# Kernel tuning notes

Measured on AMD Instinct MI355X. Metric: run time of the kernel, lower is better.

The kernel has to match this reference:

```python
import jax, jax.numpy as jnp
import numpy as np

B, H, W_GRID, K = 1024, 64, 64, 10
NEG = -1e30
DIRS = ((-1, 0), (1, 0), (0, -1), (0, 1))


def _shift(x, di, dj):
    # out[..., i, j] = x[..., i+di, j+dj]; wrapped values are masked out later
    return jnp.roll(x, (-di, -dj), axis=(-2, -1))


def _valid_masks():
    ii = jnp.arange(H)[:, None]
    jj = jnp.arange(W_GRID)[None, :]
    return [(ii + di >= 0) & (ii + di < H) & (jj + dj >= 0) & (jj + dj < W_GRID)
            for di, dj in DIRS]


def setup_inputs() -> dict:
    key = jax.random.key(0)
    ks = jax.random.split(key, 8)
    walls = (jax.random.uniform(ks[0], (B, H, W_GRID)) < 0.2).astype(jnp.float32)
    aidx = jax.random.randint(ks[1], (B,), 0, H * W_GRID)
    agent = jnp.zeros((B, H * W_GRID), jnp.float32).at[jnp.arange(B), aidx].set(1.0)
    agent = agent.reshape(B, H, W_GRID)
    goal = (jax.random.uniform(ks[2], (B, H, W_GRID)) < 0.02).astype(jnp.float32)
    obs = jnp.stack([walls, agent, goal], axis=-1)  # [B,H,W,3]
    W_phi = jax.random.normal(ks[3], (3, 3), jnp.float32) * 0.5
    b_phi = jnp.zeros((3,), jnp.float32)
    W1 = jax.random.normal(ks[4], (36, 256), jnp.float32) / np.float32(np.sqrt(36.0))
    b1 = jnp.zeros((256,), jnp.float32)
    W2 = jax.random.normal(ks[5], (256, 256), jnp.float32) / np.float32(16.0)
    b2 = jnp.zeros((256,), jnp.float32)
    W_logits = jax.random.normal(ks[6], (256, 5), jnp.float32) * 0.01
    b_logits = jnp.zeros((5,), jnp.float32)
    return {"obs": obs, "W_phi": W_phi, "b_phi": b_phi, "W1": W1, "b1": b1,
            "W2": W2, "b2": b2, "W_logits": W_logits, "b_logits": b_logits}


def _forward(obs, W_phi, b_phi, W1, b1, W2, b2, W_logits, b_logits):
    # Phi: per-cell 3->3 linear + relu (original detaches phi before VP_nn)
    phi = jax.nn.relu(jnp.einsum('bhwc,cd->bhwd', obs, W_phi) + b_phi)
    phi = jax.lax.stop_gradient(phi)
    p, rin, rout = phi[..., 0], phi[..., 1], phi[..., 2]  # each [B,H,W]
    masks = _valid_masks()
    rin_sh = [_shift(rin, di, dj) for di, dj in DIRS]

    def step(v, _):
        best = v
        for m, rs, (di, dj) in zip(masks, rin_sh, DIRS):
            nv = p * _shift(v, di, dj) + rs - rout
            best = jnp.maximum(best, jnp.where(m, nv, NEG))
        return best, None

    v0 = jnp.zeros((B, H, W_GRID), phi.dtype)
    v, _ = jax.lax.scan(step, v0, None, length=K)  # final value map [B,H,W]

    # agent position = first nonzero / argmax of channel 1
    w_ch = 1.0 - obs[..., 0]  # forward flips wall channel before neighborhood
    a_ch = obs[..., 1]
    g_ch = obs[..., 2]
    flat = jnp.argmax(a_ch.reshape(B, -1), axis=1)
    r = flat // W_GRID
    c = flat % W_GRID

    def window(x, rr, cc):
        xp = jnp.pad(x, ((1, 1), (1, 1)))
        return jax.lax.dynamic_slice(xp, (rr, cc), (3, 3)).reshape(9)

    def per_sample(wc, ac, gc, vc, rr, cc):
        return jnp.concatenate([window(wc, rr, cc), window(ac, rr, cc),
                                window(gc, rr, cc), window(vc, rr, cc)])

    feats = jax.vmap(per_sample)(w_ch, a_ch, g_ch, v, r, c)  # [B,36]

    # hidden SlimFCs have activation_fn=None (linear), per SlimFC defaults
    h = feats @ W1 + b1
    h = h @ W2 + b2
    return h @ W_logits + b_logits  # [B,5]


def reference(obs, W_phi, b_phi, W1, b1, W2, b2, W_logits, b_logits):
    return _forward(obs, W_phi, b_phi, W1, b1, W2, b2, W_logits, b_logits)
```

## Files before the change

kernel.cpp:

```cpp
#include <hip/hip_runtime.h>


#define K_ITERS 10

__device__ __forceinline__ float shr1(float x) {
    return __int_as_float(__builtin_amdgcn_mov_dpp(__float_as_int(x), 0x138, 0xF, 0xF, true));
}
__device__ __forceinline__ float shl1(float x) {
    return __int_as_float(__builtin_amdgcn_mov_dpp(__float_as_int(x), 0x130, 0xF, 0xF, true));
}
__device__ __forceinline__ float max3(float a, float b, float c) {
    return fmaxf(fmaxf(a, b), c);
}

__global__ __launch_bounds__(512) void vin_fused_kernel(
    const float* __restrict__ obs,
    const float* __restrict__ W_phi,
    const float* __restrict__ b_phi,
    const float* __restrict__ W1,
    const float* __restrict__ b1,
    const float* __restrict__ W2,
    const float* __restrict__ b2,
    const float* __restrict__ Wl,
    const float* __restrict__ bl,
    float* __restrict__ out)
{
    const int b   = blockIdx.x;
    const int tid = threadIdx.x;
    const int w   = tid >> 6;
    const int l   = tid & 63;

    __shared__ float v_s[64 * 64];
    __shared__ float bndU[2][9][64];
    __shared__ float bndD[2][9][64];
    __shared__ float rbU[9][64];
    __shared__ float rbD[9][64];
    __shared__ int   agent_pos;
    __shared__ float f_s[36];
    __shared__ float part_s[2][256];
    __shared__ __align__(16) float h1_s[256];
    __shared__ float h2_s[256];
    __shared__ float red[8][5];

    const float* ob = obs + (size_t)b * (4096 * 3);

    const float w00 = W_phi[0], w01 = W_phi[1], w02 = W_phi[2];
    const float w10 = W_phi[3], w11 = W_phi[4], w12 = W_phi[5];
    const float w20 = W_phi[6], w21 = W_phi[7], w22 = W_phi[8];
    const float bp0 = b_phi[0], bp1 = b_phi[1], bp2 = b_phi[2];

    float pk[8], rik[8], rok[8];
    #pragma unroll
    for (int k = 0; k < 8; ++k) {
        const int cell = (8 * w + k) * 64 + l;
        const float o0 = ob[cell * 3 + 0];
        const float o1 = ob[cell * 3 + 1];
        const float o2 = ob[cell * 3 + 2];
        pk[k]  = fmaxf(fmaf(o2, w20, fmaf(o1, w10, fmaf(o0, w00, bp0))), 0.f);
        rik[k] = fmaxf(fmaf(o2, w21, fmaf(o1, w11, fmaf(o0, w01, bp1))), 0.f);
        rok[k] = fmaxf(fmaf(o2, w22, fmaf(o1, w12, fmaf(o0, w02, bp2))), 0.f);
        if (o1 > 0.5f) agent_pos = cell;
    }
    const float p0 = pk[0], p1 = pk[1], p2 = pk[2], p3 = pk[3];
    const float p4 = pk[4], p5 = pk[5], p6 = pk[6], p7 = pk[7];

    if (tid < 64) {
        bndU[0][0][l] = 0.f; bndU[1][0][l] = 0.f;
        bndD[0][8][l] = 0.f; bndD[1][8][l] = 0.f;
        rbU[0][l] = 0.f;     rbD[8][l] = 0.f;
    }
    rbU[w + 1][l] = rik[7];
    rbD[w][l]     = rik[0];
    __syncthreads();
    const float rinU_b = rbU[w][l];
    const float rinD_b = rbD[w + 1][l];

    const float aU0 = rinU_b - rok[0], aU1 = rik[0] - rok[1], aU2 = rik[1] - rok[2], aU3 = rik[2] - rok[3];
    const float aU4 = rik[3] - rok[4], aU5 = rik[4] - rok[5], aU6 = rik[5] - rok[6], aU7 = rik[6] - rok[7];
    const float aD0 = rik[1] - rok[0], aD1 = rik[2] - rok[1], aD2 = rik[3] - rok[2], aD3 = rik[4] - rok[3];
    const float aD4 = rik[5] - rok[4], aD5 = rik[6] - rok[5], aD6 = rik[7] - rok[6], aD7 = rinD_b - rok[7];
    const float aL0 = shr1(rik[0]) - rok[0], aL1 = shr1(rik[1]) - rok[1], aL2 = shr1(rik[2]) - rok[2], aL3 = shr1(rik[3]) - rok[3];
    const float aL4 = shr1(rik[4]) - rok[4], aL5 = shr1(rik[5]) - rok[5], aL6 = shr1(rik[6]) - rok[6], aL7 = shr1(rik[7]) - rok[7];
    const float aR0 = shl1(rik[0]) - rok[0], aR1 = shl1(rik[1]) - rok[1], aR2 = shl1(rik[2]) - rok[2], aR3 = shl1(rik[3]) - rok[3];
    const float aR4 = shl1(rik[4]) - rok[4], aR5 = shl1(rik[5]) - rok[5], aR6 = shl1(rik[6]) - rok[6], aR7 = shl1(rik[7]) - rok[7];

    float v0 = fmaxf(max3(aU0, aD0, aL0), fmaxf(aR0, 0.f));
    float v1 = fmaxf(max3(aU1, aD1, aL1), fmaxf(aR1, 0.f));
    float v2 = fmaxf(max3(aU2, aD2, aL2), fmaxf(aR2, 0.f));
    float v3 = fmaxf(max3(aU3, aD3, aL3), fmaxf(aR3, 0.f));
    float v4 = fmaxf(max3(aU4, aD4, aL4), fmaxf(aR4, 0.f));
    float v5 = fmaxf(max3(aU5, aD5, aL5), fmaxf(aR5, 0.f));
    float v6 = fmaxf(max3(aU6, aD6, aL6), fmaxf(aR6, 0.f));
    float v7 = fmaxf(max3(aU7, aD7, aL7), fmaxf(aR7, 0.f));
    bndU[0][w + 1][l] = v7;
    bndD[0][w][l]     = v0;

    #pragma unroll
    for (int it = 1; it < K_ITERS; ++it) {
        const int rd = (it - 1) & 1, wr = it & 1;
        __syncthreads();
        const float vU_b = bndU[rd][w][l];
        const float vD_b = bndD[rd][w + 1][l];

        float vL, vR, m;
        vL = shr1(v7); vR = shl1(v7);
        m = max3(fmaf(p7, v6, aU7), fmaf(p7, vD_b, aD7), fmaf(p7, vL, aL7));
        const float nv7 = max3(m, fmaf(p7, vR, aR7), v7);
        bndU[wr][w + 1][l] = nv7;

        vL = shr1(v0); vR = shl1(v0);
        m = max3(fmaf(p0, vU_b, aU0), fmaf(p0, v1, aD0), fmaf(p0, vL, aL0));
        const float nv0 = max3(m, fmaf(p0, vR, aR0), v0);
        bndD[wr][w][l] = nv0;

        vL = shr1(v1); vR = shl1(v1);
        m = max3(fmaf(p1, v0, aU1), fmaf(p1, v2, aD1), fmaf(p1, vL, aL1));
        const float nv1 = max3(m, fmaf(p1, vR, aR1), v1);

        vL = shr1(v2); vR = shl1(v2);
        m = max3(fmaf(p2, v1, aU2), fmaf(p2, v3, aD2), fmaf(p2, vL, aL2));
        const float nv2 = max3(m, fmaf(p2, vR, aR2), v2);

        vL = shr1(v3); vR = shl1(v3);
        m = max3(fmaf(p3, v2, aU3), fmaf(p3, v4, aD3), fmaf(p3, vL, aL3));
        const float nv3 = max3(m, fmaf(p3, vR, aR3), v3);

        vL = shr1(v4); vR = shl1(v4);
        m = max3(fmaf(p4, v3, aU4), fmaf(p4, v5, aD4), fmaf(p4, vL, aL4));
        const float nv4 = max3(m, fmaf(p4, vR, aR4), v4);

        vL = shr1(v5); vR = shl1(v5);
        m = max3(fmaf(p5, v4, aU5), fmaf(p5, v6, aD5), fmaf(p5, vL, aL5));
        const float nv5 = max3(m, fmaf(p5, vR, aR5), v5);

        vL = shr1(v6); vR = shl1(v6);
        m = max3(fmaf(p6, v5, aU6), fmaf(p6, v7, aD6), fmaf(p6, vL, aL6));
        const float nv6 = max3(m, fmaf(p6, vR, aR6), v6);

        v0 = nv0; v1 = nv1; v2 = nv2; v3 = nv3;
        v4 = nv4; v5 = nv5; v6 = nv6; v7 = nv7;
    }

    v_s[(8 * w + 0) * 64 + l] = v0;
    v_s[(8 * w + 1) * 64 + l] = v1;
    v_s[(8 * w + 2) * 64 + l] = v2;
    v_s[(8 * w + 3) * 64 + l] = v3;
    v_s[(8 * w + 4) * 64 + l] = v4;
    v_s[(8 * w + 5) * 64 + l] = v5;
    v_s[(8 * w + 6) * 64 + l] = v6;
    v_s[(8 * w + 7) * 64 + l] = v7;
    __syncthreads();

    if (tid < 36) {
        const int ap = agent_pos;
        const int ar = ap >> 6, ac = ap & 63;
        const int g  = tid / 9, o = tid % 9;
        const int rr = ar + o / 3 - 1;
        const int cc = ac + o % 3 - 1;
        float val = 0.f;
        if (rr >= 0 && rr < 64 && cc >= 0 && cc < 64) {
            const int cell = rr * 64 + cc;
            if      (g == 0) val = 1.f - ob[cell * 3 + 0];
            else if (g == 1) val = ob[cell * 3 + 1];
            else if (g == 2) val = ob[cell * 3 + 2];
            else             val = v_s[cell];
        }
        f_s[tid] = val;
    }
    __syncthreads();

    {
        const int h = tid >> 8;
        const int c = tid & 255;
        float a = 0.f;
        #pragma unroll
        for (int m = 0; m < 18; ++m) {
            const int i = 18 * h + m;
            a = fmaf(f_s[i], W1[i * 256 + c], a);
        }
        part_s[h][c] = a;
    }
    __syncthreads();
    if (tid < 256) h1_s[tid] = b1[tid] + part_s[0][tid] + part_s[1][tid];
    __syncthreads();

    {
        const int h = tid >> 8;
        const int c = tid & 255;
        float a = 0.f;
        #pragma unroll
        for (int m4 = 0; m4 < 32; ++m4) {
            const int i = 128 * h + m4 * 4;
            const float4 hv = *reinterpret_cast<const float4*>(&h1_s[i]);
            a = fmaf(hv.x, W2[(i + 0) * 256 + c], a);
            a = fmaf(hv.y, W2[(i + 1) * 256 + c], a);
            a = fmaf(hv.z, W2[(i + 2) * 256 + c], a);
            a = fmaf(hv.w, W2[(i + 3) * 256 + c], a);
        }
        part_s[h][c] = a;
    }
    __syncthreads();
    if (tid < 256) h2_s[tid] = b2[tid] + part_s[0][tid] + part_s[1][tid];
    __syncthreads();

    if (tid < 40) {
        const int j  = tid % 5;
        const int ch = tid / 5;
        float acc = 0.f;
        #pragma unroll
        for (int m = 0; m < 32; ++m) {
            const int i = ch * 32 + m;
            acc = fmaf(h2_s[i], Wl[i * 5 + j], acc);
        }
        red[ch][j] = acc;
    }
    __syncthreads();
    if (tid < 5) {
        float o = bl[tid];
        #pragma unroll
        for (int ch = 0; ch < 8; ++ch) o += red[ch][tid];
        out[b * 5 + tid] = o;
    }
}

extern "C" void kernel_launch(void* const* d_in, const int* in_sizes, int n_in,
                              void* d_out, int out_size, void* d_ws, size_t ws_size,
                              hipStream_t stream) {
    const float* obs   = (const float*)d_in[0];
    const float* W_phi = (const float*)d_in[1];
    const float* b_phi = (const float*)d_in[2];
    const float* W1    = (const float*)d_in[3];
    const float* b1    = (const float*)d_in[4];
    const float* W2    = (const float*)d_in[5];
    const float* b2    = (const float*)d_in[6];
    const float* Wl    = (const float*)d_in[7];
    const float* bl    = (const float*)d_in[8];
    float* out = (float*)d_out;

    vin_fused_kernel<<<dim3(1024), dim3(512), 0, stream>>>(
        obs, W_phi, b_phi, W1, b1, W2, b2, Wl, bl, out);
}
```

Baseline: 28.46 us.

## Process two samples per block to amortize MLP weight loads and prefetch obs

Each block now handles two batch samples: the second sample's observations are loaded into registers before running value iteration on the first, and both samples share a single pass over W1 and W2 in the MLP with 2x2 register blocking. The aim is to halve global weight traffic per sample and overlap observation loads with compute. The grid drops to 512 blocks, which lowers parallelism across CUs, makes each block's value-iteration phase serial over two samples, and adds register pressure from the 24 prefetched values.

```diff
diff --git a/kernel.cpp b/kernel.cpp
--- a/kernel.cpp
+++ b/kernel.cpp
@@ -13,7 +13,99 @@
     return fmaxf(fmaxf(a, b), c);
 }
 
-__global__ __launch_bounds__(512) void vin_fused_kernel(
+__device__ __forceinline__ void vi_sample(
+    const float* __restrict__ pk, const float* __restrict__ rik,
+    const float* __restrict__ rok, int w, int l,
+    float (&bndU)[2][9][64], float (&bndD)[2][9][64],
+    float (&rbU)[9][64], float (&rbD)[9][64],
+    float* __restrict__ v_s)
+{
+    rbU[w + 1][l] = rik[7];
+    rbD[w][l]     = rik[0];
+    __syncthreads();
+    const float rinU_b = rbU[w][l];
+    const float rinD_b = rbD[w + 1][l];
+
+    const float p0 = pk[0], p1 = pk[1], p2 = pk[2], p3 = pk[3];
+    const float p4 = pk[4], p5 = pk[5], p6 = pk[6], p7 = pk[7];
+
+    const float aU0 = rinU_b - rok[0], aU1 = rik[0] - rok[1], aU2 = rik[1] - rok[2], aU3 = rik[2] - rok[3];
+    const float aU4 = rik[3] - rok[4], aU5 = rik[4] - rok[5], aU6 = rik[5] - rok[6], aU7 = rik[6] - rok[7];
+    const float aD0 = rik[1] - rok[0], aD1 = rik[2] - rok[1], aD2 = rik[3] - rok[2], aD3 = rik[4] - rok[3];
+    const float aD4 = rik[5] - rok[4], aD5 = rik[6] - rok[5], aD6 = rik[7] - rok[6], aD7 = rinD_b - rok[7];
+    const float aL0 = shr1(rik[0]) - rok[0], aL1 = shr1(rik[1]) - rok[1], aL2 = shr1(rik[2]) - rok[2], aL3 = shr1(rik[3]) - rok[3];
+    const float aL4 = shr1(rik[4]) - rok[4], aL5 = shr1(rik[5]) - rok[5], aL6 = shr1(rik[6]) - rok[6], aL7 = shr1(rik[7]) - rok[7];
+    const float aR0 = shl1(rik[0]) - rok[0], aR1 = shl1(rik[1]) - rok[1], aR2 = shl1(rik[2]) - rok[2], aR3 = shl1(rik[3]) - rok[3];
+    const float aR4 = shl1(rik[4]) - rok[4], aR5 = shl1(rik[5]) - rok[5], aR6 = shl1(rik[6]) - rok[6], aR7 = shl1(rik[7]) - rok[7];
+
+    float v0 = fmaxf(max3(aU0, aD0, aL0), fmaxf(aR0, 0.f));
+    float v1 = fmaxf(max3(aU1, aD1, aL1), fmaxf(aR1, 0.f));
+    float v2 = fmaxf(max3(aU2, aD2, aL2), fmaxf(aR2, 0.f));
+    float v3 = fmaxf(max3(aU3, aD3, aL3), fmaxf(aR3, 0.f));
+    float v4 = fmaxf(max3(aU4, aD4, aL4), fmaxf(aR4, 0.f));
+    float v5 = fmaxf(max3(aU5, aD5, aL5), fmaxf(aR5, 0.f));
+    float v6 = fmaxf(max3(aU6, aD6, aL6), fmaxf(aR6, 0.f));
+    float v7 = fmaxf(max3(aU7, aD7, aL7), fmaxf(aR7, 0.f));
+    bndU[0][w + 1][l] = v7;
+    bndD[0][w][l]     = v0;
+
+    #pragma unroll
+    for (int it = 1; it < K_ITERS; ++it) {
+        const int rd = (it - 1) & 1, wr = it & 1;
+        __syncthreads();
+        const float vU_b = bndU[rd][w][l];
+        const float vD_b = bndD[rd][w + 1][l];
+
+        float vL, vR, m;
+        vL = shr1(v7); vR = shl1(v7);
+        m = max3(fmaf(p7, v6, aU7), fmaf(p7, vD_b, aD7), fmaf(p7, vL, aL7));
+        const float nv7 = max3(m, fmaf(p7, vR, aR7), v7);
+        bndU[wr][w + 1][l] = nv7;
+
+        vL = shr1(v0); vR = shl1(v0);
+        m = max3(fmaf(p0, vU_b, aU0), fmaf(p0, v1, aD0), fmaf(p0, vL, aL0));
+        const float nv0 = max3(m, fmaf(p0, vR, aR0), v0);
+        bndD[wr][w][l] = nv0;
+
+        vL = shr1(v1); vR = shl1(v1);
+        m = max3(fmaf(p1, v0, aU1), fmaf(p1, v2, aD1), fmaf(p1, vL, aL1));
+        const float nv1 = max3(m, fmaf(p1, vR, aR1), v1);
+
+        vL = shr1(v2); vR = shl1(v2);
+        m = max3(fmaf(p2, v1, aU2), fmaf(p2, v3, aD2), fmaf(p2, vL, aL2));
+        const float nv2 = max3(m, fmaf(p2, vR, aR2), v2);
+
+        vL = shr1(v3); vR = shl1(v3);
+        m = max3(fmaf(p3, v2, aU3), fmaf(p3, v4, aD3), fmaf(p3, vL, aL3));
+        const float nv3 = max3(m, fmaf(p3, vR, aR3), v3);
+
+        vL = shr1(v4); vR = shl1(v4);
+        m = max3(fmaf(p4, v3, aU4), fmaf(p4, v5, aD4), fmaf(p4, vL, aL4));
+        const float nv4 = max3(m, fmaf(p4, vR, aR4), v4);
+
+        vL = shr1(v5); vR = shl1(v5);
+        m = max3(fmaf(p5, v4, aU5), fmaf(p5, v6, aD5), fmaf(p5, vL, aL5));
+        const float nv5 = max3(m, fmaf(p5, vR, aR5), v5);
+
+        vL = shr1(v6); vR = shl1(v6);
+        m = max3(fmaf(p6, v5, aU6), fmaf(p6, v7, aD6), fmaf(p6, vL, aL6));
+        const float nv6 = max3(m, fmaf(p6, vR, aR6), v6);
+
+        v0 = nv0; v1 = nv1; v2 = nv2; v3 = nv3;
+        v4 = nv4; v5 = nv5; v6 = nv6; v7 = nv7;
+    }
+
+    v_s[(8 * w + 0) * 64 + l] = v0;
+    v_s[(8 * w + 1) * 64 + l] = v1;
+    v_s[(8 * w + 2) * 64 + l] = v2;
+    v_s[(8 * w + 3) * 64 + l] = v3;
+    v_s[(8 * w + 4) * 64 + l] = v4;
+    v_s[(8 * w + 5) * 64 + l] = v5;
+    v_s[(8 * w + 6) * 64 + l] = v6;
+    v_s[(8 * w + 7) * 64 + l] = v7;
+}
+
+__global__ __launch_bounds__(512) void vin_fused2_kernel(
     const float* __restrict__ obs,
     const float* __restrict__ W_phi,
     const float* __restrict__ b_phi,
@@ -25,134 +117,63 @@
     const float* __restrict__ bl,
     float* __restrict__ out)
 {
-    const int b   = blockIdx.x;
+    const int bA  = blockIdx.x;
+    const int bB  = blockIdx.x + 512;
     const int tid = threadIdx.x;
     const int w   = tid >> 6;
     const int l   = tid & 63;
 
     __shared__ float v_s[64 * 64];
-    __shared__ float bndU[2][9][64];
-    __shared__ float bndD[2][9][64];
-    __shared__ float rbU[9][64];
-    __shared__ float rbD[9][64];
-    __shared__ int   agent_pos;
-    __shared__ float f_s[36];
-    __shared__ float part_s[2][256];
-    __shared__ __align__(16) float h1_s[256];
-    __shared__ float h2_s[256];
-    __shared__ float red[8][5];
-
-    const float* ob = obs + (size_t)b * (4096 * 3);
+    __shared__ float bndU[2][9][64], bndD[2][9][64];
+    __shared__ float rbU[9][64], rbD[9][64];
+    __shared__ int   agent_pos[2];
+    __shared__ float f_s[2][36];
+    __shared__ __align__(16) float part_s[4][2][256];
+    __shared__ __align__(16) float h1_s[256][2];
+    __shared__ float h2_s[2][256];
+    __shared__ float red[8][2][5];
+
+    const float* obA = obs + (size_t)bA * 12288;
+    const float* obB = obs + (size_t)bB * 12288;
 
     const float w00 = W_phi[0], w01 = W_phi[1], w02 = W_phi[2];
     const float w10 = W_phi[3], w11 = W_phi[4], w12 = W_phi[5];
     const float w20 = W_phi[6], w21 = W_phi[7], w22 = W_phi[8];
     const float bp0 = b_phi[0], bp1 = b_phi[1], bp2 = b_phi[2];
 
-    float pk[8], rik[8], rok[8];
-    #pragma unroll
-    for (int k = 0; k < 8; ++k) {
-        const int cell = (8 * w + k) * 64 + l;
-        const float o0 = ob[cell * 3 + 0];
-        const float o1 = ob[cell * 3 + 1];
-        const float o2 = ob[cell * 3 + 2];
-        pk[k]  = fmaxf(fmaf(o2, w20, fmaf(o1, w10, fmaf(o0, w00, bp0))), 0.f);
-        rik[k] = fmaxf(fmaf(o2, w21, fmaf(o1, w11, fmaf(o0, w01, bp1))), 0.f);
-        rok[k] = fmaxf(fmaf(o2, w22, fmaf(o1, w12, fmaf(o0, w02, bp2))), 0.f);
-        if (o1 > 0.5f) agent_pos = cell;
-    }
-    const float p0 = pk[0], p1 = pk[1], p2 = pk[2], p3 = pk[3];
-    const float p4 = pk[4], p5 = pk[5], p6 = pk[6], p7 = pk[7];
-
     if (tid < 64) {
         bndU[0][0][l] = 0.f; bndU[1][0][l] = 0.f;
         bndD[0][8][l] = 0.f; bndD[1][8][l] = 0.f;
         rbU[0][l] = 0.f;     rbD[8][l] = 0.f;
     }
-    rbU[w + 1][l] = rik[7];
-    rbD[w][l]     = rik[0];
-    __syncthreads();
-    const float rinU_b = rbU[w][l];
-    const float rinD_b = rbD[w + 1][l];
-
-    const float aU0 = rinU_b - rok[0], aU1 = rik[0] - rok[1], aU2 = rik[1] - rok[2], aU3 = rik[2] - rok[3];
-    const float aU4 = rik[3] - rok[4], aU5 = rik[4] - rok[5], aU6 = rik[5] - rok[6], aU7 = rik[6] - rok[7];
-    const float aD0 = rik[1] - rok[0], aD1 = rik[2] - rok[1], aD2 = rik[3] - rok[2], aD3 = rik[4] - rok[3];
-    const float aD4 = rik[5] - rok[4], aD5 = rik[6] - rok[5], aD6 = rik[7] - rok[6], aD7 = rinD_b - rok[7];
-    const float aL0 = shr1(rik[0]) - rok[0], aL1 = shr1(rik[1]) - rok[1], aL2 = shr1(rik[2]) - rok[2], aL3 = shr1(rik[3]) - rok[3];
-    const float aL4 = shr1(rik[4]) - rok[4], aL5 = shr1(rik[5]) - rok[5], aL6 = shr1(rik[6]) - rok[6], aL7 = shr1(rik[7]) - rok[7];
-    const float aR0 = shl1(rik[0]) - rok[0], aR1 = shl1(rik[1]) - rok[1], aR2 = shl1(rik[2]) - rok[2], aR3 = shl1(rik[3]) - rok[3];
-    const float aR4 = shl1(rik[4]) - rok[4], aR5 = shl1(rik[5]) - rok[5], aR6 = shl1(rik[6]) - rok[6], aR7 = shl1(rik[7]) - rok[7];
-
-    float v0 = fmaxf(max3(aU0, aD0, aL0), fmaxf(aR0, 0.f));
-    float v1 = fmaxf(max3(aU1, aD1, aL1), fmaxf(aR1, 0.f));
-    float v2 = fmaxf(max3(aU2, aD2, aL2), fmaxf(aR2, 0.f));
-    float v3 = fmaxf(max3(aU3, aD3, aL3), fmaxf(aR3, 0.f));
-    float v4 = fmaxf(max3(aU4, aD4, aL4), fmaxf(aR4, 0.f));
-    float v5 = fmaxf(max3(aU5, aD5, aL5), fmaxf(aR5, 0.f));
-    float v6 = fmaxf(max3(aU6, aD6, aL6), fmaxf(aR6, 0.f));
-    float v7 = fmaxf(max3(aU7, aD7, aL7), fmaxf(aR7, 0.f));
-    bndU[0][w + 1][l] = v7;
-    bndD[0][w][l]     = v0;
-
+
+    float pkA[8], rikA[8], rokA[8];
     #pragma unroll
-    for (int it = 1; it < K_ITERS; ++it) {
-        const int rd = (it - 1) & 1, wr = it & 1;
-        __syncthreads();
-        const float vU_b = bndU[rd][w][l];
-        const float vD_b = bndD[rd][w + 1][l];
-
-        float vL, vR, m;
-        vL = shr1(v7); vR = shl1(v7);
-        m = max3(fmaf(p7, v6, aU7), fmaf(p7, vD_b, aD7), fmaf(p7, vL, aL7));
-        const float nv7 = max3(m, fmaf(p7, vR, aR7), v7);
-        bndU[wr][w + 1][l] = nv7;
-
-        vL = shr1(v0); vR = shl1(v0);
-        m = max3(fmaf(p0, vU_b, aU0), fmaf(p0, v1, aD0), fmaf(p0, vL, aL0));
-        const float nv0 = max3(m, fmaf(p0, vR, aR0), v0);
-        bndD[wr][w][l] = nv0;
-
-        vL = shr1(v1); vR = shl1(v1);
-        m = max3(fmaf(p1, v0, aU1), fmaf(p1, v2, aD1), fmaf(p1, vL, aL1));
-        const float nv1 = max3(m, fmaf(p1, vR, aR1), v1);
-
-        vL = shr1(v2); vR = shl1(v2);
-        m = max3(fmaf(p2, v1, aU2), fmaf(p2, v3, aD2), fmaf(p2, vL, aL2));
-        const float nv2 = max3(m, fmaf(p2, vR, aR2), v2);
-
-        vL = shr1(v3); vR = shl1(v3);
-        m = max3(fmaf(p3, v2, aU3), fmaf(p3, v4, aD3), fmaf(p3, vL, aL3));
-        const float nv3 = max3(m, fmaf(p3, vR, aR3), v3);
-
-        vL = shr1(v4); vR = shl1(v4);
-        m = max3(fmaf(p4, v3, aU4), fmaf(p4, v5, aD4), fmaf(p4, vL, aL4));
-        const float nv4 = max3(m, fmaf(p4, vR, aR4), v4);
-
-        vL = shr1(v5); vR = shl1(v5);
-        m = max3(fmaf(p5, v4, aU5), fmaf(p5, v6, aD5), fmaf(p5, vL, aL5));
-        const float nv5 = max3(m, fmaf(p5, vR, aR5), v5);
-
-        vL = shr1(v6); vR = shl1(v6);
-        m = max3(fmaf(p6, v5, aU6), fmaf(p6, v7, aD6), fmaf(p6, vL, aL6));
-        const float nv6 = max3(m, fmaf(p6, vR, aR6), v6);
-
-        v0 = nv0; v1 = nv1; v2 = nv2; v3 = nv3;
-        v4 = nv4; v5 = nv5; v6 = nv6; v7 = nv7;
-    }
-
-    v_s[(8 * w + 0) * 64 + l] = v0;
-    v_s[(8 * w + 1) * 64 + l] = v1;
-    v_s[(8 * w + 2) * 64 + l] = v2;
-    v_s[(8 * w + 3) * 64 + l] = v3;
-    v_s[(8 * w + 4) * 64 + l] = v4;
-    v_s[(8 * w + 5) * 64 + l] = v5;
-    v_s[(8 * w + 6) * 64 + l] = v6;
-    v_s[(8 * w + 7) * 64 + l] = v7;
+    for (int k = 0; k < 8; ++k) {
+        const int cell = (8 * w + k) * 64 + l;
+        const float o0 = obA[cell * 3 + 0];
+        const float o1 = obA[cell * 3 + 1];
+        const float o2 = obA[cell * 3 + 2];
+        pkA[k]  = fmaxf(fmaf(o2, w20, fmaf(o1, w10, fmaf(o0, w00, bp0))), 0.f);
+        rikA[k] = fmaxf(fmaf(o2, w21, fmaf(o1, w11, fmaf(o0, w01, bp1))), 0.f);
+        rokA[k] = fmaxf(fmaf(o2, w22, fmaf(o1, w12, fmaf(o0, w02, bp2))), 0.f);
+        if (o1 > 0.5f) agent_pos[0] = cell;
+    }
+
+    float oB[24];
+    #pragma unroll
+    for (int k = 0; k < 8; ++k) {
+        const int cell = (8 * w + k) * 64 + l;
+        oB[3 * k + 0] = obB[cell * 3 + 0];
+        oB[3 * k + 1] = obB[cell * 3 + 1];
+        oB[3 * k + 2] = obB[cell * 3 + 2];
+    }
+
+    vi_sample(pkA, rikA, rokA, w, l, bndU, bndD, rbU, rbD, v_s);
     __syncthreads();
 
     if (tid < 36) {
-        const int ap = agent_pos;
+        const int ap = agent_pos[0];
         const int ar = ap >> 6, ac = ap & 63;
         const int g  = tid / 9, o = tid % 9;
         const int rr = ar + o / 3 - 1;
@@ -160,66 +181,115 @@
         float val = 0.f;
         if (rr >= 0 && rr < 64 && cc >= 0 && cc < 64) {
             const int cell = rr * 64 + cc;
-            if      (g == 0) val = 1.f - ob[cell * 3 + 0];
-            else if (g == 1) val = ob[cell * 3 + 1];
-            else if (g == 2) val = ob[cell * 3 + 2];
+            if      (g == 0) val = 1.f - obA[cell * 3 + 0];
+            else if (g == 1) val = obA[cell * 3 + 1];
+            else if (g == 2) val = obA[cell * 3 + 2];
             else             val = v_s[cell];
         }
-        f_s[tid] = val;
+        f_s[0][tid] = val;
+    }
+
+    float pkB[8], rikB[8], rokB[8];
+    #pragma unroll
+    for (int k = 0; k < 8; ++k) {
+        const int cell = (8 * w + k) * 64 + l;
+        const float o0 = oB[3 * k + 0];
+        const float o1 = oB[3 * k + 1];
+        const float o2 = oB[3 * k + 2];
+        pkB[k]  = fmaxf(fmaf(o2, w20, fmaf(o1, w10, fmaf(o0, w00, bp0))), 0.f);
+        rikB[k] = fmaxf(fmaf(o2, w21, fmaf(o1, w11, fmaf(o0, w01, bp1))), 0.f);
+        rokB[k] = fmaxf(fmaf(o2, w22, fmaf(o1, w12, fmaf(o0, w02, bp2))), 0.f);
+        if (o1 > 0.5f) agent_pos[1] = cell;
+    }
+    vi_sample(pkB, rikB, rokB, w, l, bndU, bndD, rbU, rbD, v_s);
+    __syncthreads();
+
+    if (tid < 36) {
+        const int ap = agent_pos[1];
+        const int ar = ap >> 6, ac = ap & 63;
+        const int g  = tid / 9, o = tid % 9;
+        const int rr = ar + o / 3 - 1;
+        const int cc = ac + o % 3 - 1;
+        float val = 0.f;
+        if (rr >= 0 && rr < 64 && cc >= 0 && cc < 64) {
+            const int cell = rr * 64 + cc;
+            if      (g == 0) val = 1.f - obB[cell * 3 + 0];
+            else if (g == 1) val = obB[cell * 3 + 1];
+            else if (g == 2) val = obB[cell * 3 + 2];
+            else             val = v_s[cell];
+        }
+        f_s[1][tid] = val;
     }
     __syncthreads();
 
     {
-        const int h = tid >> 8;
-        const int c = tid & 255;
-        float a = 0.f;
+        const int q  = tid >> 7;
+        const int cp = tid & 127;
+        float a00 = 0.f, a01 = 0.f, a10 = 0.f, a11 = 0.f;
         #pragma unroll
-        for (int m = 0; m < 18; ++m) {
-            const int i = 18 * h + m;
-            a = fmaf(f_s[i], W1[i * 256 + c], a);
-        }
-        part_s[h][c] = a;
-    }
-    __syncthreads();
-    if (tid < 256) h1_s[tid] = b1[tid] + part_s[0][tid] + part_s[1][tid];
-    __syncthreads();
-
+        for (int m = 0; m < 9; ++m) {
+            const int i = 9 * q + m;
+            const float2 wv = *reinterpret_cast<const float2*>(&W1[i * 256 + 2 * cp]);
+            const float fA = f_s[0][i], fB = f_s[1][i];
+            a00 = fmaf(fA, wv.x, a00); a01 = fmaf(fA, wv.y, a01);
+            a10 = fmaf(fB, wv.x, a10); a11 = fmaf(fB, wv.y, a11);
+        }
+        *reinterpret_cast<float2*>(&part_s[q][0][2 * cp]) = make_float2(a00, a01);
+        *reinterpret_cast<float2*>(&part_s[q][1][2 * cp]) = make_float2(a10, a11);
+    }
+    __syncthreads();
     {
-        const int h = tid >> 8;
-        const int c = tid & 255;
-        float a = 0.f;
+        const int s = tid >> 8, c = tid & 255;
+        h1_s[c][s] = b1[c] + ((part_s[0][s][c] + part_s[1][s][c]) +
+                              (part_s[2][s][c] + part_s[3][s][c]));
+    }
+    __syncthreads();
+
+    {
+        const int q  = tid >> 7;
+        const int cp = tid & 127;
+        float a00 = 0.f, a01 = 0.f, a10 = 0.f, a11 = 0.f;
         #pragma unroll
-        for (int m4 = 0; m4 < 32; ++m4) {
-            const int i = 128 * h + m4 * 4;
-            const float4 hv = *reinterpret_cast<const float4*>(&h1_s[i]);
-            a = fmaf(hv.x, W2[(i + 0) * 256 + c], a);
-            a = fmaf(hv.y, W2[(i + 1) * 256 + c], a);
-            a = fmaf(hv.z, W2[(i + 2) * 256 + c], a);
-            a = fmaf(hv.w, W2[(i + 3) * 256 + c], a);
-        }
-        part_s[h][c] = a;
-    }
-    __syncthreads();
-    if (tid < 256) h2_s[tid] = b2[tid] + part_s[0][tid] + part_s[1][tid];
-    __syncthreads();
-
-    if (tid < 40) {
-        const int j  = tid % 5;
-        const int ch = tid / 5;
+        for (int m2 = 0; m2 < 32; ++m2) {
+            const int i = 64 * q + 2 * m2;
+            const float4 hv = *reinterpret_cast<const float4*>(&h1_s[i][0]);
+            const float2 w0 = *reinterpret_cast<const float2*>(&W2[i * 256 + 2 * cp]);
+            const float2 w1 = *reinterpret_cast<const float2*>(&W2[(i + 1) * 256 + 2 * cp]);
+            a00 = fmaf(hv.x, w0.x, a00); a01 = fmaf(hv.x, w0.y, a01);
+            a10 = fmaf(hv.y, w0.x, a10); a11 = fmaf(hv.y, w0.y, a11);
+            a00 = fmaf(hv.z, w1.x, a00); a01 = fmaf(hv.z, w1.y, a01);
+            a10 = fmaf(hv.w, w1.x, a10); a11 = fmaf(hv.w, w1.y, a11);
+        }
+        *reinterpret_cast<float2*>(&part_s[q][0][2 * cp]) = make_float2(a00, a01);
+        *reinterpret_cast<float2*>(&part_s[q][1][2 * cp]) = make_float2(a10, a11);
+    }
+    __syncthreads();
+    {
+        const int s = tid >> 8, c = tid & 255;
+        h2_s[s][c] = b2[c] + ((part_s[0][s][c] + part_s[1][s][c]) +
+                              (part_s[2][s][c] + part_s[3][s][c]));
+    }
+    __syncthreads();
+
+    if (tid < 80) {
+        const int s  = tid & 1;
+        const int j  = (tid >> 1) % 5;
+        const int ch = tid / 10;
         float acc = 0.f;
         #pragma unroll
         for (int m = 0; m < 32; ++m) {
             const int i = ch * 32 + m;
-            acc = fmaf(h2_s[i], Wl[i * 5 + j], acc);
-        }
-        red[ch][j] = acc;
-    }
-    __syncthreads();
-    if (tid < 5) {
-        float o = bl[tid];
+            acc = fmaf(h2_s[s][i], Wl[i * 5 + j], acc);
+        }
+        red[ch][s][j] = acc;
+    }
+    __syncthreads();
+    if (tid < 10) {
+        const int s = tid & 1, j = tid >> 1;
+        float o = bl[j];
         #pragma unroll
-        for (int ch = 0; ch < 8; ++ch) o += red[ch][tid];
-        out[b * 5 + tid] = o;
+        for (int ch = 0; ch < 8; ++ch) o += red[ch][s][j];
+        out[(s ? bB : bA) * 5 + j] = o;
     }
 }
 
@@ -237,6 +307,6 @@
     const float* bl    = (const float*)d_in[8];
     float* out = (float*)d_out;
 
-    vin_fused_kernel<<<dim3(1024), dim3(512), 0, stream>>>(
+    vin_fused2_kernel<<<dim3(512), dim3(512), 0, stream>>>(
         obs, W_phi, b_phi, W1, b1, W2, b2, Wl, bl, out);
 }
```

New measurement: 31.31 us. +10.0%, slower.

## Process two samples per block to share MLP weight loads

Applied to the files above, without the earlier changes.

Each 1024-thread block now handles two batch samples, running the value-iteration stencil for each in its own 512-thread half. The MLP layers load each W1/W2 weight once and apply it to both samples using interleaved shared-memory activations, which halves global weight traffic per sample. The cost is that the two halves now share every __syncthreads, so one sample's iterations can stall the other, and the grid drops to 512 blocks, which lowers occupancy flexibility.

```diff
diff --git a/kernel.cpp b/kernel.cpp
--- a/kernel.cpp
+++ b/kernel.cpp
@@ -13,7 +13,99 @@
     return fmaxf(fmaxf(a, b), c);
 }
 
-__global__ __launch_bounds__(512) void vin_fused_kernel(
+__device__ __forceinline__ void vi_sample(
+    const float* __restrict__ pk, const float* __restrict__ rik,
+    const float* __restrict__ rok, int w, int l,
+    float (&bndU)[2][9][64], float (&bndD)[2][9][64],
+    float (&rbU)[9][64], float (&rbD)[9][64],
+    float* __restrict__ v_s)
+{
+    rbU[w + 1][l] = rik[7];
+    rbD[w][l]     = rik[0];
+    __syncthreads();
+    const float rinU_b = rbU[w][l];
+    const float rinD_b = rbD[w + 1][l];
+
+    const float p0 = pk[0], p1 = pk[1], p2 = pk[2], p3 = pk[3];
+    const float p4 = pk[4], p5 = pk[5], p6 = pk[6], p7 = pk[7];
+
+    const float aU0 = rinU_b - rok[0], aU1 = rik[0] - rok[1], aU2 = rik[1] - rok[2], aU3 = rik[2] - rok[3];
+    const float aU4 = rik[3] - rok[4], aU5 = rik[4] - rok[5], aU6 = rik[5] - rok[6], aU7 = rik[6] - rok[7];
+    const float aD0 = rik[1] - rok[0], aD1 = rik[2] - rok[1], aD2 = rik[3] - rok[2], aD3 = rik[4] - rok[3];
+    const float aD4 = rik[5] - rok[4], aD5 = rik[6] - rok[5], aD6 = rik[7] - rok[6], aD7 = rinD_b - rok[7];
+    const float aL0 = shr1(rik[0]) - rok[0], aL1 = shr1(rik[1]) - rok[1], aL2 = shr1(rik[2]) - rok[2], aL3 = shr1(rik[3]) - rok[3];
+    const float aL4 = shr1(rik[4]) - rok[4], aL5 = shr1(rik[5]) - rok[5], aL6 = shr1(rik[6]) - rok[6], aL7 = shr1(rik[7]) - rok[7];
+    const float aR0 = shl1(rik[0]) - rok[0], aR1 = shl1(rik[1]) - rok[1], aR2 = shl1(rik[2]) - rok[2], aR3 = shl1(rik[3]) - rok[3];
+    const float aR4 = shl1(rik[4]) - rok[4], aR5 = shl1(rik[5]) - rok[5], aR6 = shl1(rik[6]) - rok[6], aR7 = shl1(rik[7]) - rok[7];
+
+    float v0 = fmaxf(max3(aU0, aD0, aL0), fmaxf(aR0, 0.f));
+    float v1 = fmaxf(max3(aU1, aD1, aL1), fmaxf(aR1, 0.f));
+    float v2 = fmaxf(max3(aU2, aD2, aL2), fmaxf(aR2, 0.f));
+    float v3 = fmaxf(max3(aU3, aD3, aL3), fmaxf(aR3, 0.f));
+    float v4 = fmaxf(max3(aU4, aD4, aL4), fmaxf(aR4, 0.f));
+    float v5 = fmaxf(max3(aU5, aD5, aL5), fmaxf(aR5, 0.f));
+    float v6 = fmaxf(max3(aU6, aD6, aL6), fmaxf(aR6, 0.f));
+    float v7 = fmaxf(max3(aU7, aD7, aL7), fmaxf(aR7, 0.f));
+    bndU[0][w + 1][l] = v7;
+    bndD[0][w][l]     = v0;
+
+    #pragma unroll
+    for (int it = 1; it < K_ITERS; ++it) {
+        const int rd = (it - 1) & 1, wr = it & 1;
+        __syncthreads();
+        const float vU_b = bndU[rd][w][l];
+        const float vD_b = bndD[rd][w + 1][l];
+
+        float vL, vR, m;
+        vL = shr1(v7); vR = shl1(v7);
+        m = max3(fmaf(p7, v6, aU7), fmaf(p7, vD_b, aD7), fmaf(p7, vL, aL7));
+        const float nv7 = max3(m, fmaf(p7, vR, aR7), v7);
+        bndU[wr][w + 1][l] = nv7;
+
+        vL = shr1(v0); vR = shl1(v0);
+        m = max3(fmaf(p0, vU_b, aU0), fmaf(p0, v1, aD0), fmaf(p0, vL, aL0));
+        const float nv0 = max3(m, fmaf(p0, vR, aR0), v0);
+        bndD[wr][w][l] = nv0;
+
+        vL = shr1(v1); vR = shl1(v1);
+        m = max3(fmaf(p1, v0, aU1), fmaf(p1, v2, aD1), fmaf(p1, vL, aL1));
+        const float nv1 = max3(m, fmaf(p1, vR, aR1), v1);
+
+        vL = shr1(v2); vR = shl1(v2);
+        m = max3(fmaf(p2, v1, aU2), fmaf(p2, v3, aD2), fmaf(p2, vL, aL2));
+        const float nv2 = max3(m, fmaf(p2, vR, aR2), v2);
+
+        vL = shr1(v3); vR = shl1(v3);
+        m = max3(fmaf(p3, v2, aU3), fmaf(p3, v4, aD3), fmaf(p3, vL, aL3));
+        const float nv3 = max3(m, fmaf(p3, vR, aR3), v3);
+
+        vL = shr1(v4); vR = shl1(v4);
+        m = max3(fmaf(p4, v3, aU4), fmaf(p4, v5, aD4), fmaf(p4, vL, aL4));
+        const float nv4 = max3(m, fmaf(p4, vR, aR4), v4);
+
+        vL = shr1(v5); vR = shl1(v5);
+        m = max3(fmaf(p5, v4, aU5), fmaf(p5, v6, aD5), fmaf(p5, vL, aL5));
+        const float nv5 = max3(m, fmaf(p5, vR, aR5), v5);
+
+        vL = shr1(v6); vR = shl1(v6);
+        m = max3(fmaf(p6, v5, aU6), fmaf(p6, v7, aD6), fmaf(p6, vL, aL6));
+        const float nv6 = max3(m, fmaf(p6, vR, aR6), v6);
+
+        v0 = nv0; v1 = nv1; v2 = nv2; v3 = nv3;
+        v4 = nv4; v5 = nv5; v6 = nv6; v7 = nv7;
+    }
+
+    v_s[(8 * w + 0) * 64 + l] = v0;
+    v_s[(8 * w + 1) * 64 + l] = v1;
+    v_s[(8 * w + 2) * 64 + l] = v2;
+    v_s[(8 * w + 3) * 64 + l] = v3;
+    v_s[(8 * w + 4) * 64 + l] = v4;
+    v_s[(8 * w + 5) * 64 + l] = v5;
+    v_s[(8 * w + 6) * 64 + l] = v6;
+    v_s[(8 * w + 7) * 64 + l] = v7;
+}
+
+__global__ __launch_bounds__(1024) void vin_fused2c_kernel(
     const float* __restrict__ obs,
     const float* __restrict__ W_phi,
     const float* __restrict__ b_phi,
@@ -25,24 +117,25 @@
     const float* __restrict__ bl,
     float* __restrict__ out)
 {
-    const int b   = blockIdx.x;
     const int tid = threadIdx.x;
-    const int w   = tid >> 6;
-    const int l   = tid & 63;
-
-    __shared__ float v_s[64 * 64];
-    __shared__ float bndU[2][9][64];
-    __shared__ float bndD[2][9][64];
-    __shared__ float rbU[9][64];
-    __shared__ float rbD[9][64];
-    __shared__ int   agent_pos;
-    __shared__ float f_s[36];
-    __shared__ float part_s[2][256];
-    __shared__ __align__(16) float h1_s[256];
-    __shared__ float h2_s[256];
-    __shared__ float red[8][5];
-
-    const float* ob = obs + (size_t)b * (4096 * 3);
+    const int s   = tid >> 9;
+    const int st  = tid & 511;
+    const int w   = st >> 6;
+    const int l   = st & 63;
+    const int b   = blockIdx.x + s * 512;
+
+    __shared__ float v_s[2][4096];
+    __shared__ float bndU[2][2][9][64];
+    __shared__ float bndD[2][2][9][64];
+    __shared__ float rbU[2][9][64], rbD[2][9][64];
+    __shared__ int   agent_pos[2];
+    __shared__ __align__(8)  float f_s[36][2];
+    __shared__ float part_s[4][2][256];
+    __shared__ __align__(16) float h1_s[256][2];
+    __shared__ float h2_s[2][256];
+    __shared__ float red[8][2][5];
+
+    const float* ob = obs + (size_t)b * 12288;
 
     const float w00 = W_phi[0], w01 = W_phi[1], w02 = W_phi[2];
     const float w10 = W_phi[3], w11 = W_phi[4], w12 = W_phi[5];
@@ -59,102 +152,22 @@
         pk[k]  = fmaxf(fmaf(o2, w20, fmaf(o1, w10, fmaf(o0, w00, bp0))), 0.f);
         rik[k] = fmaxf(fmaf(o2, w21, fmaf(o1, w11, fmaf(o0, w01, bp1))), 0.f);
         rok[k] = fmaxf(fmaf(o2, w22, fmaf(o1, w12, fmaf(o0, w02, bp2))), 0.f);
-        if (o1 > 0.5f) agent_pos = cell;
-    }
-    const float p0 = pk[0], p1 = pk[1], p2 = pk[2], p3 = pk[3];
-    const float p4 = pk[4], p5 = pk[5], p6 = pk[6], p7 = pk[7];
-
-    if (tid < 64) {
-        bndU[0][0][l] = 0.f; bndU[1][0][l] = 0.f;
-        bndD[0][8][l] = 0.f; bndD[1][8][l] = 0.f;
-        rbU[0][l] = 0.f;     rbD[8][l] = 0.f;
-    }
-    rbU[w + 1][l] = rik[7];
-    rbD[w][l]     = rik[0];
-    __syncthreads();
-    const float rinU_b = rbU[w][l];
-    const float rinD_b = rbD[w + 1][l];
-
-    const float aU0 = rinU_b - rok[0], aU1 = rik[0] - rok[1], aU2 = rik[1] - rok[2], aU3 = rik[2] - rok[3];
-    const float aU4 = rik[3] - rok[4], aU5 = rik[4] - rok[5], aU6 = rik[5] - rok[6], aU7 = rik[6] - rok[7];
-    const float aD0 = rik[1] - rok[0], aD1 = rik[2] - rok[1], aD2 = rik[3] - rok[2], aD3 = rik[4] - rok[3];
-    const float aD4 = rik[5] - rok[4], aD5 = rik[6] - rok[5], aD6 = rik[7] - rok[6], aD7 = rinD_b - rok[7];
-    const float aL0 = shr1(rik[0]) - rok[0], aL1 = shr1(rik[1]) - rok[1], aL2 = shr1(rik[2]) - rok[2], aL3 = shr1(rik[3]) - rok[3];
-    const float aL4 = shr1(rik[4]) - rok[4], aL5 = shr1(rik[5]) - rok[5], aL6 = shr1(rik[6]) - rok[6], aL7 = shr1(rik[7]) - rok[7];
-    const float aR0 = shl1(rik[0]) - rok[0], aR1 = shl1(rik[1]) - rok[1], aR2 = shl1(rik[2]) - rok[2], aR3 = shl1(rik[3]) - rok[3];
-    const float aR4 = shl1(rik[4]) - rok[4], aR5 = shl1(rik[5]) - rok[5], aR6 = shl1(rik[6]) - rok[6], aR7 = shl1(rik[7]) - rok[7];
-
-    float v0 = fmaxf(max3(aU0, aD0, aL0), fmaxf(aR0, 0.f));
-    float v1 = fmaxf(max3(aU1, aD1, aL1), fmaxf(aR1, 0.f));
-    float v2 = fmaxf(max3(aU2, aD2, aL2), fmaxf(aR2, 0.f));
-    float v3 = fmaxf(max3(aU3, aD3, aL3), fmaxf(aR3, 0.f));
-    float v4 = fmaxf(max3(aU4, aD4, aL4), fmaxf(aR4, 0.f));
-    float v5 = fmaxf(max3(aU5, aD5, aL5), fmaxf(aR5, 0.f));
-    float v6 = fmaxf(max3(aU6, aD6, aL6), fmaxf(aR6, 0.f));
-    float v7 = fmaxf(max3(aU7, aD7, aL7), fmaxf(aR7, 0.f));
-    bndU[0][w + 1][l] = v7;
-    bndD[0][w][l]     = v0;
-
-    #pragma unroll
-    for (int it = 1; it < K_ITERS; ++it) {
-        const int rd = (it - 1) & 1, wr = it & 1;
-        __syncthreads();
-        const float vU_b = bndU[rd][w][l];
-        const float vD_b = bndD[rd][w + 1][l];
-
-        float vL, vR, m;
-        vL = shr1(v7); vR = shl1(v7);
-        m = max3(fmaf(p7, v6, aU7), fmaf(p7, vD_b, aD7), fmaf(p7, vL, aL7));
-        const float nv7 = max3(m, fmaf(p7, vR, aR7), v7);
-        bndU[wr][w + 1][l] = nv7;
-
-        vL = shr1(v0); vR = shl1(v0);
-        m = max3(fmaf(p0, vU_b, aU0), fmaf(p0, v1, aD0), fmaf(p0, vL, aL0));
-        const float nv0 = max3(m, fmaf(p0, vR, aR0), v0);
-        bndD[wr][w][l] = nv0;
-
-        vL = shr1(v1); vR = shl1(v1);
-        m = max3(fmaf(p1, v0, aU1), fmaf(p1, v2, aD1), fmaf(p1, vL, aL1));
-        const float nv1 = max3(m, fmaf(p1, vR, aR1), v1);
-
-        vL = shr1(v2); vR = shl1(v2);
-        m = max3(fmaf(p2, v1, aU2), fmaf(p2, v3, aD2), fmaf(p2, vL, aL2));
-        const float nv2 = max3(m, fmaf(p2, vR, aR2), v2);
-
-        vL = shr1(v3); vR = shl1(v3);
-        m = max3(fmaf(p3, v2, aU3), fmaf(p3, v4, aD3), fmaf(p3, vL, aL3));
-        const float nv3 = max3(m, fmaf(p3, vR, aR3), v3);
-
-        vL = shr1(v4); vR = shl1(v4);
-        m = max3(fmaf(p4, v3, aU4), fmaf(p4, v5, aD4), fmaf(p4, vL, aL4));
-        const float nv4 = max3(m, fmaf(p4, vR, aR4), v4);
-
-        vL = shr1(v5); vR = shl1(v5);
-        m = max3(fmaf(p5, v4, aU5), fmaf(p5, v6, aD5), fmaf(p5, vL, aL5));
-        const float nv5 = max3(m, fmaf(p5, vR, aR5), v5);
-
-        vL = shr1(v6); vR = shl1(v6);
-        m = max3(fmaf(p6, v5, aU6), fmaf(p6, v7, aD6), fmaf(p6, vL, aL6));
-        const float nv6 = max3(m, fmaf(p6, vR, aR6), v6);
-
-        v0 = nv0; v1 = nv1; v2 = nv2; v3 = nv3;
-        v4 = nv4; v5 = nv5; v6 = nv6; v7 = nv7;
-    }
-
-    v_s[(8 * w + 0) * 64 + l] = v0;
-    v_s[(8 * w + 1) * 64 + l] = v1;
-    v_s[(8 * w + 2) * 64 + l] = v2;
-    v_s[(8 * w + 3) * 64 + l] = v3;
-    v_s[(8 * w + 4) * 64 + l] = v4;
-    v_s[(8 * w + 5) * 64 + l] = v5;
-    v_s[(8 * w + 6) * 64 + l] = v6;
-    v_s[(8 * w + 7) * 64 + l] = v7;
-    __syncthreads();
-
-    if (tid < 36) {
-        const int ap = agent_pos;
+        if (o1 > 0.5f) agent_pos[s] = cell;
+    }
+
+    if (st < 64) {
+        bndU[s][0][0][l] = 0.f; bndU[s][1][0][l] = 0.f;
+        bndD[s][0][8][l] = 0.f; bndD[s][1][8][l] = 0.f;
+        rbU[s][0][l] = 0.f;     rbD[s][8][l] = 0.f;
+    }
+
+    vi_sample(pk, rik, rok, w, l, bndU[s], bndD[s], rbU[s], rbD[s], v_s[s]);
+    __syncthreads();
+
+    if (st < 36) {
+        const int ap = agent_pos[s];
         const int ar = ap >> 6, ac = ap & 63;
-        const int g  = tid / 9, o = tid % 9;
+        const int g  = st / 9, o = st % 9;
         const int rr = ar + o / 3 - 1;
         const int cc = ac + o % 3 - 1;
         float val = 0.f;
@@ -163,63 +176,80 @@
             if      (g == 0) val = 1.f - ob[cell * 3 + 0];
             else if (g == 1) val = ob[cell * 3 + 1];
             else if (g == 2) val = ob[cell * 3 + 2];
-            else             val = v_s[cell];
-        }
-        f_s[tid] = val;
+            else             val = v_s[s][cell];
+        }
+        f_s[st][s] = val;
     }
     __syncthreads();
 
     {
-        const int h = tid >> 8;
+        const int q = tid >> 8;
         const int c = tid & 255;
-        float a = 0.f;
-        #pragma unroll
-        for (int m = 0; m < 18; ++m) {
-            const int i = 18 * h + m;
-            a = fmaf(f_s[i], W1[i * 256 + c], a);
-        }
-        part_s[h][c] = a;
-    }
-    __syncthreads();
-    if (tid < 256) h1_s[tid] = b1[tid] + part_s[0][tid] + part_s[1][tid];
+        float a0 = 0.f, a1 = 0.f;
+        #pragma unroll
+        for (int m = 0; m < 9; ++m) {
+            const int i = 9 * q + m;
+            const float wv = W1[i * 256 + c];
+            const float2 fv = *reinterpret_cast<const float2*>(&f_s[i][0]);
+            a0 = fmaf(fv.x, wv, a0);
+            a1 = fmaf(fv.y, wv, a1);
+        }
+        part_s[q][0][c] = a0;
+        part_s[q][1][c] = a1;
+    }
+    __syncthreads();
+    if (tid < 512) {
+        const int ss = tid >> 8, c = tid & 255;
+        h1_s[c][ss] = b1[c] + ((part_s[0][ss][c] + part_s[1][ss][c]) +
+                               (part_s[2][ss][c] + part_s[3][ss][c]));
+    }
     __syncthreads();
 
     {
-        const int h = tid >> 8;
+        const int q = tid >> 8;
         const int c = tid & 255;
-        float a = 0.f;
-        #pragma unroll
-        for (int m4 = 0; m4 < 32; ++m4) {
-            const int i = 128 * h + m4 * 4;
-            const float4 hv = *reinterpret_cast<const float4*>(&h1_s[i]);
-            a = fmaf(hv.x, W2[(i + 0) * 256 + c], a);
-            a = fmaf(hv.y, W2[(i + 1) * 256 + c], a);
-            a = fmaf(hv.z, W2[(i + 2) * 256 + c], a);
-            a = fmaf(hv.w, W2[(i + 3) * 256 + c], a);
-        }
-        part_s[h][c] = a;
-    }
-    __syncthreads();
-    if (tid < 256) h2_s[tid] = b2[tid] + part_s[0][tid] + part_s[1][tid];
-    __syncthreads();
-
-    if (tid < 40) {
-        const int j  = tid % 5;
-        const int ch = tid / 5;
+        float a0 = 0.f, a1 = 0.f;
+        #pragma unroll
+        for (int m2 = 0; m2 < 32; ++m2) {
+            const int i = 64 * q + 2 * m2;
+            const float4 hv = *reinterpret_cast<const float4*>(&h1_s[i][0]);
+            const float wv0 = W2[(i + 0) * 256 + c];
+            const float wv1 = W2[(i + 1) * 256 + c];
+            a0 = fmaf(hv.x, wv0, a0);
+            a1 = fmaf(hv.y, wv0, a1);
+            a0 = fmaf(hv.z, wv1, a0);
+            a1 = fmaf(hv.w, wv1, a1);
+        }
+        part_s[q][0][c] = a0;
+        part_s[q][1][c] = a1;
+    }
+    __syncthreads();
+    if (tid < 512) {
+        const int ss = tid >> 8, c = tid & 255;
+        h2_s[ss][c] = b2[c] + ((part_s[0][ss][c] + part_s[1][ss][c]) +
+                               (part_s[2][ss][c] + part_s[3][ss][c]));
+    }
+    __syncthreads();
+
+    if (tid < 80) {
+        const int ss = tid & 1;
+        const int j  = (tid >> 1) % 5;
+        const int ch = tid / 10;
         float acc = 0.f;
         #pragma unroll
         for (int m = 0; m < 32; ++m) {
             const int i = ch * 32 + m;
-            acc = fmaf(h2_s[i], Wl[i * 5 + j], acc);
-        }
-        red[ch][j] = acc;
-    }
-    __syncthreads();
-    if (tid < 5) {
-        float o = bl[tid];
-        #pragma unroll
-        for (int ch = 0; ch < 8; ++ch) o += red[ch][tid];
-        out[b * 5 + tid] = o;
+            acc = fmaf(h2_s[ss][i], Wl[i * 5 + j], acc);
+        }
+        red[ch][ss][j] = acc;
+    }
+    __syncthreads();
+    if (tid < 10) {
+        const int ss = tid & 1, j = tid >> 1;
+        float o = bl[j];
+        #pragma unroll
+        for (int ch = 0; ch < 8; ++ch) o += red[ch][ss][j];
+        out[(blockIdx.x + ss * 512) * 5 + j] = o;
     }
 }
 
@@ -237,6 +267,6 @@
     const float* bl    = (const float*)d_in[8];
     float* out = (float*)d_out;
 
-    vin_fused_kernel<<<dim3(1024), dim3(512), 0, stream>>>(
+    vin_fused2c_kernel<<<dim3(512), dim3(1024), 0, stream>>>(
         obs, W_phi, b_phi, W1, b1, W2, b2, Wl, bl, out);
 }
```

Result: faster. 27.49 us (-3.4%).
